# Optimization experiments

Hardware: AMD Instinct MI355X
Metric: run time of the kernel (lower is better)

## Reference

```python
import jax, jax.numpy as jnp
import numpy as np

NEG_SLOPE = 0.01  # torch F.leaky_relu default


def setup_inputs() -> dict:
    key = jax.random.key(0)
    k1, k2, k3, k4 = jax.random.split(key, 4)
    B, N, F_in, F_out = 16, 2048, 128, 128
    stdv = 1.0 / np.sqrt(F_out)
    h = jax.random.normal(k1, (B, N, F_in), dtype=jnp.float32)
    adj = jax.random.uniform(k2, (B, N, N), dtype=jnp.float32)
    W = jax.random.uniform(k3, (F_in, F_out), minval=-stdv, maxval=stdv, dtype=jnp.float32)
    a = jax.random.uniform(k4, (2 * F_out, 1), minval=-stdv, maxval=stdv, dtype=jnp.float32)
    return {"h": h, "adj": adj, "W": W, "a": a}


def reference(h, adj, W, a):
    # Wh: [B, N, F_out]
    Wh = jnp.matmul(h, W)
    F_out = W.shape[1]
    a1 = a[:F_out, 0]  # [F_out]
    a2 = a[F_out:, 0]  # [F_out]
    # concat-score factorizes: e[b,i,j] = leaky(Wh[b,i]@a1 + Wh[b,j]@a2)
    f1 = jnp.einsum('bnf,f->bn', Wh, a1)  # [B, N]
    f2 = jnp.einsum('bnf,f->bn', Wh, a2)  # [B, N]
    e = jax.nn.leaky_relu(f1[:, :, None] + f2[:, None, :], negative_slope=NEG_SLOPE)  # [B,N,N]
    # NOTE: original softmax is over dim=1 (row index i), faithfully preserved
    attention = jax.nn.softmax(e, axis=1)
    h_prime = jnp.einsum('bij,bjf->bif', attention, Wh)  # bmm
    return h_prime
```

## Files before the change

kernel.cpp:

```cpp
#include <hip/hip_runtime.h>

#define BB 16
#define NN 2048
#define FF 128
#define NEG 0.01f
#define CH 128
#define CL (NN / CH)

__global__ __launch_bounds__(256) void k_wh(const float* __restrict__ h,
                                            const float* __restrict__ Wg,
                                            const float* __restrict__ a,
                                            float* __restrict__ Wh,
                                            float* __restrict__ f1,
                                            float* __restrict__ f2) {
    __shared__ float Ws[64 * 128];
    __shared__ float hsT[64 * 36];

    const int tid  = threadIdx.x;
    const int fg   = tid & 31;
    const int slot = tid >> 5;
    const int f4   = fg * 4;
    const int rowBase = blockIdx.x * 32;

    float acc[4][4];
#pragma unroll
    for (int r = 0; r < 4; ++r)
#pragma unroll
        for (int c = 0; c < 4; ++c) acc[r][c] = 0.f;

    const float4* Wg4 = (const float4*)Wg;
    const float4* hg4 = (const float4*)h;

    for (int kh = 0; kh < 128; kh += 64) {
        __syncthreads();
        for (int idx = tid; idx < 64 * 32; idx += 256) {
            int kk = idx >> 5, ff = idx & 31;
            ((float4*)Ws)[kk * 32 + ff] = Wg4[(size_t)(kh + kk) * 32 + ff];
        }
#pragma unroll
        for (int pass = 0; pass < 2; ++pass) {
            int idx = pass * 256 + tid;
            int kq = idx & 15, row = idx >> 4;
            float4 h4 = hg4[(size_t)(rowBase + row) * 32 + (kh >> 2) + kq];
            hsT[(kq * 4 + 0) * 36 + row] = h4.x;
            hsT[(kq * 4 + 1) * 36 + row] = h4.y;
            hsT[(kq * 4 + 2) * 36 + row] = h4.z;
            hsT[(kq * 4 + 3) * 36 + row] = h4.w;
        }
        __syncthreads();
#pragma unroll 8
        for (int kk = 0; kk < 64; ++kk) {
            float4 wv = *(const float4*)&Ws[kk * 128 + f4];
            float4 hv = *(const float4*)&hsT[kk * 36 + slot * 4];
            acc[0][0] += hv.x * wv.x; acc[0][1] += hv.x * wv.y; acc[0][2] += hv.x * wv.z; acc[0][3] += hv.x * wv.w;
            acc[1][0] += hv.y * wv.x; acc[1][1] += hv.y * wv.y; acc[1][2] += hv.y * wv.z; acc[1][3] += hv.y * wv.w;
            acc[2][0] += hv.z * wv.x; acc[2][1] += hv.z * wv.y; acc[2][2] += hv.z * wv.z; acc[2][3] += hv.z * wv.w;
            acc[3][0] += hv.w * wv.x; acc[3][1] += hv.w * wv.y; acc[3][2] += hv.w * wv.z; acc[3][3] += hv.w * wv.w;
        }
    }

    const float4* ag4 = (const float4*)a;
    float4 a1v = ag4[fg];
    float4 a2v = ag4[32 + fg];

#pragma unroll
    for (int r = 0; r < 4; ++r) {
        int row = rowBase + slot * 4 + r;
        float4 o; o.x = acc[r][0]; o.y = acc[r][1]; o.z = acc[r][2]; o.w = acc[r][3];
        *(float4*)&Wh[(size_t)row * 128 + f4] = o;
        float p1 = acc[r][0] * a1v.x + acc[r][1] * a1v.y + acc[r][2] * a1v.z + acc[r][3] * a1v.w;
        float p2 = acc[r][0] * a2v.x + acc[r][1] * a2v.y + acc[r][2] * a2v.z + acc[r][3] * a2v.w;
#pragma unroll
        for (int m = 16; m >= 1; m >>= 1) {
            p1 += __shfl_xor(p1, m);
            p2 += __shfl_xor(p2, m);
        }
        if (fg == 0) { f1[row] = p1; f2[row] = p2; }
    }
}

__device__ __forceinline__ float wave_incl_scan(float s, int lane) {
#pragma unroll
    for (int m = 1; m <= 32; m <<= 1) {
        float o = __shfl_up(s, m);
        if (lane >= m) s += o;
    }
    return s;
}

template<bool WITHIDX>
__device__ __forceinline__ void cex_shfl(float& v0, float& v1, int& i0, int& i1,
                                         int tid, int j, int k) {
    const int  pj    = j >> 1;
    const bool islow = ((tid & pj) == 0);
    const bool up    = (((tid << 1) & k) == 0);
    float o0 = __shfl_xor(v0, pj);
    float o1 = __shfl_xor(v1, pj);
    int oi0 = 0, oi1 = 0;
    if (WITHIDX) { oi0 = __shfl_xor(i0, pj); oi1 = __shfl_xor(i1, pj); }
    {
        float vl = islow ? v0 : o0, vu = islow ? o0 : v0;
        if ((vl > vu) == up) { v0 = o0; if (WITHIDX) i0 = oi0; }
    }
    {
        float vl = islow ? v1 : o1, vu = islow ? o1 : v1;
        if ((vl > vu) == up) { v1 = o1; if (WITHIDX) i1 = oi1; }
    }
}

template<bool WITHIDX>
__device__ __forceinline__ void cex_intra(float& v0, float& v1, int& i0, int& i1,
                                          int tid, int k) {
    const bool up = (((tid << 1) & k) == 0);
    if ((v0 > v1) == up) {
        float tv = v0; v0 = v1; v1 = tv;
        if (WITHIDX) { int ti = i0; i0 = i1; i1 = ti; }
    }
}

template<bool WITHIDX>
__device__ __forceinline__ void bitonic2048(float* sKey, int* sIdx,
                                            float v0, float v1, int i0, int i1,
                                            int tid) {
#pragma unroll
    for (int k = 2; k <= 128; k <<= 1) {
#pragma unroll
        for (int j = 64; j >= 2; j >>= 1)
            if (j <= (k >> 1)) cex_shfl<WITHIDX>(v0, v1, i0, i1, tid, j, k);
        cex_intra<WITHIDX>(v0, v1, i0, i1, tid, k);
    }
    sKey[2 * tid] = v0; sKey[2 * tid + 1] = v1;
    if (WITHIDX) { sIdx[2 * tid] = i0; sIdx[2 * tid + 1] = i1; }

    for (int k = 256; k <= NN; k <<= 1) {
        for (int j = k >> 1; j >= 128; j >>= 1) {
            __syncthreads();
            int mask = j - 1;
            int i   = ((tid & ~mask) << 1) | (tid & mask);
            int ixj = i | j;
            bool up = ((i & k) == 0);
            float av = sKey[i], bv = sKey[ixj];
            if ((av > bv) == up) {
                sKey[i] = bv; sKey[ixj] = av;
                if (WITHIDX) { int t2 = sIdx[i]; sIdx[i] = sIdx[ixj]; sIdx[ixj] = t2; }
            }
        }
        __syncthreads();
        v0 = sKey[2 * tid]; v1 = sKey[2 * tid + 1];
        if (WITHIDX) { i0 = sIdx[2 * tid]; i1 = sIdx[2 * tid + 1]; }
#pragma unroll
        for (int j = 64; j >= 2; j >>= 1) cex_shfl<WITHIDX>(v0, v1, i0, i1, tid, j, k);
        cex_intra<WITHIDX>(v0, v1, i0, i1, tid, k);
        sKey[2 * tid] = v0; sKey[2 * tid + 1] = v1;
        if (WITHIDX) { sIdx[2 * tid] = i0; sIdx[2 * tid + 1] = i1; }
    }
}

__global__ __launch_bounds__(1024) void k_sort2(const float* __restrict__ f1,
                                                const float* __restrict__ f2,
                                                float* __restrict__ SF1g,
                                                float* __restrict__ PAg,
                                                float* __restrict__ SAg,
                                                float* __restrict__ SKg,
                                                int* __restrict__ PERM,
                                                int* __restrict__ KIDX,
                                                int* __restrict__ ROWS,
                                                int* __restrict__ BOFF) {
    __shared__ float sKey[NN];
    __shared__ int   sIdx[NN];
    __shared__ float wtot[16];
    __shared__ int   hist[CH];
    __shared__ int   hscan[CH + 1];
    __shared__ int   sbuf[CH];

    const int tid  = threadIdx.x;
    const int lane = tid & 63;
    const int w    = tid >> 6;
    const int b    = blockIdx.x & 15;
    const int task = blockIdx.x >> 4;

    const float* f1b = f1 + b * NN;
    const float* f2b = f2 + b * NN;

    if (task == 0) {
        float2 p = ((const float2*)f1b)[tid];
        int i0 = 0, i1 = 0;
        bitonic2048<false>(sKey, sIdx, p.x, p.y, i0, i1, tid);
    } else {
        float2 p = ((const float2*)f2b)[tid];
        bitonic2048<true>(sKey, sIdx, p.x, p.y, 2 * tid, 2 * tid + 1, tid);
    }
    __syncthreads();

    if (task == 0) {
        for (int i = tid; i < NN; i += 1024) SF1g[b * NN + i] = sKey[i];
        const size_t pbase = (size_t)b * (NN + 1);
        {
            float a0 = expf(NEG * sKey[2 * tid]);
            float a1 = expf(NEG * sKey[2 * tid + 1]);
            float s = a0 + a1;
            float v = wave_incl_scan(s, lane);
            if (lane == 63) wtot[w] = v;
            __syncthreads();
            float off = 0.f;
#pragma unroll
            for (int ww = 0; ww < 16; ++ww) off += (ww < w) ? wtot[ww] : 0.f;
            float excl = off + v - s;
            PAg[pbase + 2 * tid]     = excl;
            PAg[pbase + 2 * tid + 1] = excl + a0;
            if (tid == 1023) PAg[pbase + NN] = off + v;
        }
        __syncthreads();
        {
            float y0 = expf(sKey[NN - 1 - 2 * tid]);
            float y1 = expf(sKey[NN - 2 - 2 * tid]);
            float s = y0 + y1;
            float v = wave_incl_scan(s, lane);
            if (lane == 63) wtot[w] = v;
            __syncthreads();
            float off = 0.f;
#pragma unroll
            for (int ww = 0; ww < 16; ++ww) off += (ww < w) ? wtot[ww] : 0.f;
            SAg[pbase + NN - 1 - 2 * tid] = off + (v - s) + y0;
            SAg[pbase + NN - 2 - 2 * tid] = off + v;
            if (tid == 0) SAg[pbase + NN] = 0.f;
        }
    } else {
        for (int i = tid; i < NN; i += 1024) {
            SKg[b * NN + i]  = sKey[i];
            PERM[b * NN + i] = sIdx[i];
        }
        if (tid < CH) hist[tid] = 0;
        __syncthreads();
        for (int i = tid; i < NN; i += 1024) {
            float tau = -f1b[i];
            int lo = 0, hi = NN;
            while (lo < hi) { int m = (lo + hi) >> 1; if (sKey[m] <= tau) lo = m + 1; else hi = m; }
            KIDX[b * NN + i] = lo;
            int c = lo / CL;
            if (c > CH - 1) c = CH - 1;
            sIdx[i] = c;
            atomicAdd(&hist[c], 1);
        }
        __syncthreads();
        if (tid < CH) sbuf[tid] = hist[tid];
        for (int off = 1; off < CH; off <<= 1) {
            __syncthreads();
            int v = 0;
            if (tid < CH) { v = sbuf[tid]; if (tid >= off) v += sbuf[tid - off]; }
            __syncthreads();
            if (tid < CH) sbuf[tid] = v;
        }
        __syncthreads();
        if (tid == 0) hscan[0] = 0;
        if (tid < CH) hscan[tid + 1] = sbuf[tid];
        __syncthreads();
        if (tid <= CH) BOFF[b * (CH + 1) + tid] = hscan[tid];
        if (tid < CH) hist[tid] = hscan[tid];
        __syncthreads();
        for (int i = tid; i < NN; i += 1024) {
            int c = sIdx[i];
            int pos = atomicAdd(&hist[c], 1);
            ROWS[b * NN + pos] = i;
        }
    }
}

__global__ __launch_bounds__(256) void k_uw(const float* __restrict__ SF1g,
                                            const float* __restrict__ PAg,
                                            const float* __restrict__ SAg,
                                            const float* __restrict__ SKg,
                                            float* __restrict__ Uarr,
                                            float* __restrict__ Warr) {
    __shared__ float sS[NN];
    __shared__ float sP[NN + 1];
    __shared__ float sA[NN + 1];
    const int b = blockIdx.x >> 3;
    const int q = blockIdx.x & 7;
    const int tid = threadIdx.x;
    const size_t pbase = (size_t)b * (NN + 1);
    for (int i = tid; i < NN; i += 256) sS[i] = SF1g[b * NN + i];
    for (int i = tid; i < NN + 1; i += 256) { sP[i] = PAg[pbase + i]; sA[i] = SAg[pbase + i]; }
    __syncthreads();
    const int t = q * 256 + tid;
    float f2v = SKg[b * NN + t];
    float tau = -f2v;
    int lo = 0, hi = NN;
    while (lo < hi) { int m = (lo + hi) >> 1; if (sS[m] <= tau) lo = m + 1; else hi = m; }
    float eS = expf(NEG * f2v);
    float eF = expf(f2v);
    float inv = 1.0f / (eS * sP[lo] + eF * sA[lo]);
    Uarr[b * NN + t] = eF * inv;
    Warr[b * NN + t] = eS * inv;
}

__global__ __launch_bounds__(128) void k_chunk(const float* __restrict__ Wh,
                                               const float* __restrict__ Uarr,
                                               const float* __restrict__ Warr,
                                               const int* __restrict__ PERM,
                                               float* __restrict__ CU,
                                               float* __restrict__ CW) {
    int blk = blockIdx.x;
    int b = blk / CH, c = blk % CH;
    int f = threadIdx.x;
    int base = b * NN + c * CL;
    const float* Whb = Wh + (size_t)b * NN * FF;
    float aU = 0.f, aW = 0.f;
#pragma unroll
    for (int t = 0; t < CL; ++t) {
        int j = PERM[base + t];
        float uv = Uarr[base + t], wv = Warr[base + t];
        float whv = Whb[(size_t)j * FF + f];
        aU += uv * whv; aW += wv * whv;
    }
    CU[(size_t)blk * FF + f] = aU;
    CW[(size_t)blk * FF + f] = aW;
}

__global__ __launch_bounds__(128) void k_offsets(float* __restrict__ CU,
                                                 float* __restrict__ CW,
                                                 float* __restrict__ TOT) {
    int b = blockIdx.x, f = threadIdx.x;
    float aU = 0.f, aW = 0.f;
#pragma unroll 8
    for (int c = 0; c < CH; ++c) {
        size_t idx = (size_t)(b * CH + c) * FF + f;
        float tU = CU[idx], tW = CW[idx];
        CU[idx] = aU; CW[idx] = aW;
        aU += tU; aW += tW;
    }
    TOT[b * FF + f] = aU;
}

__global__ __launch_bounds__(128) void k_emit(const float* __restrict__ Wh,
                                              const float* __restrict__ Uarr,
                                              const float* __restrict__ Warr,
                                              const int* __restrict__ PERM,
                                              const float* __restrict__ CU,
                                              const float* __restrict__ CW,
                                              const float* __restrict__ TOT,
                                              const float* __restrict__ f1,
                                              const int* __restrict__ KIDX,
                                              const int* __restrict__ ROWS,
                                              const int* __restrict__ BOFF,
                                              float* __restrict__ out) {
    __shared__ float pU[CL + 1][FF];
    __shared__ float pW[CL + 1][FF];

    const int blk = blockIdx.x;
    const int b = blk / CH, c = blk % CH;
    const int f = threadIdx.x;

    float aU = CU[(size_t)blk * FF + f];
    float aW = CW[(size_t)blk * FF + f];
    const float totU = TOT[b * FF + f];

    const int base = b * NN + c * CL;
    const float* Whb = Wh + (size_t)b * NN * FF;
#pragma unroll
    for (int t = 0; t < CL; ++t) {
        pU[t][f] = aU; pW[t][f] = aW;
        int j = PERM[base + t];
        float whv = Whb[(size_t)j * FF + f];
        aU += Uarr[base + t] * whv;
        aW += Warr[base + t] * whv;
    }
    pU[CL][f] = aU; pW[CL][f] = aW;
    __syncthreads();

    const int rb = BOFF[b * (CH + 1) + c];
    const int re = BOFF[b * (CH + 1) + c + 1];
    for (int idx = rb; idx < re; ++idx) {
        int i = ROWS[b * NN + idx];
        int k = KIDX[b * NN + i];
        int r = k - c * CL;
        float f1v = f1[b * NN + i];
        float alpha = expf(NEG * f1v);
        float beta  = expf(f1v);
        out[((size_t)(b * NN + i)) * FF + f] = alpha * pW[r][f] + beta * (totU - pU[r][f]);
    }
}

extern "C" void kernel_launch(void* const* d_in, const int* in_sizes, int n_in,
                              void* d_out, int out_size, void* d_ws, size_t ws_size,
                              hipStream_t stream) {
    const float* h  = (const float*)d_in[0];
    const float* W  = (const float*)d_in[2];
    const float* a  = (const float*)d_in[3];
    float* out = (float*)d_out;

    float* ws = (float*)d_ws;
    float* Wh   = ws;  ws += (size_t)BB * NN * FF;
    float* f1   = ws;  ws += BB * NN;
    float* f2   = ws;  ws += BB * NN;
    float* SF1  = ws;  ws += BB * NN;
    float* PA   = ws;  ws += BB * (NN + 1);
    float* SA   = ws;  ws += BB * (NN + 1);
    float* SK   = ws;  ws += BB * NN;
    float* Uarr = ws;  ws += BB * NN;
    float* Warr = ws;  ws += BB * NN;
    float* CU   = ws;  ws += (size_t)BB * CH * FF;
    float* CW   = ws;  ws += (size_t)BB * CH * FF;
    float* TOT  = ws;  ws += BB * FF;
    int* PERM = (int*)ws;  ws += BB * NN;
    int* KIDX = (int*)ws;  ws += BB * NN;
    int* ROWS = (int*)ws;  ws += BB * NN;
    int* BOFF = (int*)ws;

    k_wh     <<<(BB * NN) / 32, 256, 0, stream>>>(h, W, a, Wh, f1, f2);
    k_sort2  <<<2 * BB, 1024, 0, stream>>>(f1, f2, SF1, PA, SA, SK, PERM, KIDX, ROWS, BOFF);
    k_uw     <<<BB * 8, 256, 0, stream>>>(SF1, PA, SA, SK, Uarr, Warr);
    k_chunk  <<<BB * CH, 128, 0, stream>>>(Wh, Uarr, Warr, PERM, CU, CW);
    k_offsets<<<BB, 128, 0, stream>>>(CU, CW, TOT);
    k_emit   <<<BB * CH, 128, 0, stream>>>(Wh, Uarr, Warr, PERM, CU, CW, TOT, f1, KIDX, ROWS, BOFF, out);
}
```

Measured before the change: 380.9 us.

## Fuse U/W computation, chunk sums and offset scan into one kernel

Merges the per-key weight computation, the per-chunk weighted Wh sums and the chunk prefix scan into a single kernel. A per-batch atomic ticket lets the last finishing block run the scan, and the counter is reset in the sort kernel. This removes two kernel launches and the round-trip of U/W through global memory. In exchange, the chunk sums now run on far fewer blocks, each looping over eight chunks, which reduces parallelism.

Result: slower. 393.8 us (+3.4%).

```diff
diff --git a/kernel.cpp b/kernel.cpp
--- a/kernel.cpp
+++ b/kernel.cpp
@@ -165,7 +165,8 @@
                                                 int* __restrict__ PERM,
                                                 int* __restrict__ KIDX,
                                                 int* __restrict__ ROWS,
-                                                int* __restrict__ BOFF) {
+                                                int* __restrict__ BOFF,
+                                                int* __restrict__ CNT) {
     __shared__ float sKey[NN];
     __shared__ int   sIdx[NN];
     __shared__ float wtot[16];
@@ -226,6 +227,7 @@
             if (tid == 0) SAg[pbase + NN] = 0.f;
         }
     } else {
+        if (tid == 0) CNT[b] = 0;
         for (int i = tid; i < NN; i += 1024) {
             SKg[b * NN + i]  = sKey[i];
             PERM[b * NN + i] = sIdx[i];
@@ -266,22 +268,31 @@
     }
 }
 
-__global__ __launch_bounds__(256) void k_uw(const float* __restrict__ SF1g,
-                                            const float* __restrict__ PAg,
-                                            const float* __restrict__ SAg,
-                                            const float* __restrict__ SKg,
-                                            float* __restrict__ Uarr,
-                                            float* __restrict__ Warr) {
+__global__ __launch_bounds__(256) void k_uwc(const float* __restrict__ SF1g,
+                                             const float* __restrict__ PAg,
+                                             const float* __restrict__ SAg,
+                                             const float* __restrict__ SKg,
+                                             const float* __restrict__ Wh,
+                                             const int* __restrict__ PERM,
+                                             float* __restrict__ Uarr,
+                                             float* __restrict__ Warr,
+                                             float* __restrict__ CU,
+                                             float* __restrict__ CW,
+                                             float* __restrict__ TOT,
+                                             int* __restrict__ CNT) {
     __shared__ float sS[NN];
-    __shared__ float sP[NN + 1];
-    __shared__ float sA[NN + 1];
-    const int b = blockIdx.x >> 3;
-    const int q = blockIdx.x & 7;
+    __shared__ float sU[256];
+    __shared__ float sW[256];
+    __shared__ int   lastTicket;
+
+    const int b   = blockIdx.x >> 3;
+    const int q   = blockIdx.x & 7;
     const int tid = threadIdx.x;
     const size_t pbase = (size_t)b * (NN + 1);
+
     for (int i = tid; i < NN; i += 256) sS[i] = SF1g[b * NN + i];
-    for (int i = tid; i < NN + 1; i += 256) { sP[i] = PAg[pbase + i]; sA[i] = SAg[pbase + i]; }
-    __syncthreads();
+    __syncthreads();
+
     const int t = q * 256 + tid;
     float f2v = SKg[b * NN + t];
     float tau = -f2v;
@@ -289,47 +300,51 @@
     while (lo < hi) { int m = (lo + hi) >> 1; if (sS[m] <= tau) lo = m + 1; else hi = m; }
     float eS = expf(NEG * f2v);
     float eF = expf(f2v);
-    float inv = 1.0f / (eS * sP[lo] + eF * sA[lo]);
-    Uarr[b * NN + t] = eF * inv;
-    Warr[b * NN + t] = eS * inv;
-}
-
-__global__ __launch_bounds__(128) void k_chunk(const float* __restrict__ Wh,
-                                               const float* __restrict__ Uarr,
-                                               const float* __restrict__ Warr,
-                                               const int* __restrict__ PERM,
-                                               float* __restrict__ CU,
-                                               float* __restrict__ CW) {
-    int blk = blockIdx.x;
-    int b = blk / CH, c = blk % CH;
-    int f = threadIdx.x;
-    int base = b * NN + c * CL;
+    float inv = 1.0f / (eS * PAg[pbase + lo] + eF * SAg[pbase + lo]);
+    float u = eF * inv, w = eS * inv;
+    Uarr[b * NN + t] = u;
+    Warr[b * NN + t] = w;
+    sU[tid] = u; sW[tid] = w;
+    __syncthreads();
+
+    const int f = tid & 127;
+    const int g = tid >> 7;
     const float* Whb = Wh + (size_t)b * NN * FF;
-    float aU = 0.f, aW = 0.f;
-#pragma unroll
-    for (int t = 0; t < CL; ++t) {
-        int j = PERM[base + t];
-        float uv = Uarr[base + t], wv = Warr[base + t];
-        float whv = Whb[(size_t)j * FF + f];
-        aU += uv * whv; aW += wv * whv;
-    }
-    CU[(size_t)blk * FF + f] = aU;
-    CW[(size_t)blk * FF + f] = aW;
-}
-
-__global__ __launch_bounds__(128) void k_offsets(float* __restrict__ CU,
-                                                 float* __restrict__ CW,
-                                                 float* __restrict__ TOT) {
-    int b = blockIdx.x, f = threadIdx.x;
-    float aU = 0.f, aW = 0.f;
+    for (int cc = 0; cc < 8; ++cc) {
+        int lc = g * 8 + cc;
+        int c  = q * 16 + lc;
+        int tb = lc * CL;
+        int gbase = b * NN + c * CL;
+        float aU = 0.f, aW = 0.f;
+#pragma unroll
+        for (int t2 = 0; t2 < CL; ++t2) {
+            int j = PERM[gbase + t2];
+            float whv = Whb[(size_t)j * FF + f];
+            aU += sU[tb + t2] * whv;
+            aW += sW[tb + t2] * whv;
+        }
+        CU[(size_t)(b * CH + c) * FF + f] = aU;
+        CW[(size_t)(b * CH + c) * FF + f] = aW;
+    }
+
+    __threadfence();
+    __syncthreads();
+    if (tid == 0) lastTicket = atomicAdd(&CNT[b], 1);
+    __syncthreads();
+    if (lastTicket == 7) {
+        __threadfence();
+        if (tid < 128) {
+            float aU = 0.f, aW = 0.f;
 #pragma unroll 8
-    for (int c = 0; c < CH; ++c) {
-        size_t idx = (size_t)(b * CH + c) * FF + f;
-        float tU = CU[idx], tW = CW[idx];
-        CU[idx] = aU; CW[idx] = aW;
-        aU += tU; aW += tW;
-    }
-    TOT[b * FF + f] = aU;
+            for (int c = 0; c < CH; ++c) {
+                size_t idx = (size_t)(b * CH + c) * FF + f;
+                float tU = CU[idx], tW = CW[idx];
+                CU[idx] = aU; CW[idx] = aW;
+                aU += tU; aW += tW;
+            }
+            TOT[b * FF + f] = aU;
+        }
+    }
 }
 
 __global__ __launch_bounds__(128) void k_emit(const float* __restrict__ Wh,
@@ -405,12 +420,11 @@
     int* PERM = (int*)ws;  ws += BB * NN;
     int* KIDX = (int*)ws;  ws += BB * NN;
     int* ROWS = (int*)ws;  ws += BB * NN;
-    int* BOFF = (int*)ws;
-
-    k_wh     <<<(BB * NN) / 32, 256, 0, stream>>>(h, W, a, Wh, f1, f2);
-    k_sort2  <<<2 * BB, 1024, 0, stream>>>(f1, f2, SF1, PA, SA, SK, PERM, KIDX, ROWS, BOFF);
-    k_uw     <<<BB * 8, 256, 0, stream>>>(SF1, PA, SA, SK, Uarr, Warr);
-    k_chunk  <<<BB * CH, 128, 0, stream>>>(Wh, Uarr, Warr, PERM, CU, CW);
-    k_offsets<<<BB, 128, 0, stream>>>(CU, CW, TOT);
-    k_emit   <<<BB * CH, 128, 0, stream>>>(Wh, Uarr, Warr, PERM, CU, CW, TOT, f1, KIDX, ROWS, BOFF, out);
-}
+    int* BOFF = (int*)ws;  ws += BB * (CH + 1);
+    int* CNT  = (int*)ws;
+
+    k_wh    <<<(BB * NN) / 32, 256, 0, stream>>>(h, W, a, Wh, f1, f2);
+    k_sort2 <<<2 * BB, 1024, 0, stream>>>(f1, f2, SF1, PA, SA, SK, PERM, KIDX, ROWS, BOFF, CNT);
+    k_uwc   <<<BB * 8, 256, 0, stream>>>(SF1, PA, SA, SK, Wh, PERM, Uarr, Warr, CU, CW, TOT, CNT);
+    k_emit  <<<BB * CH, 128, 0, stream>>>(Wh, Uarr, Warr, PERM, CU, CW, TOT, f1, KIDX, ROWS, BOFF, out);
+}
```
